# Performance work log

Measured on AMD Instinct MI355X. Metric: run time of the kernel, lower is better.

The kernel has to match this reference:

```python
import jax, jax.numpy as jnp
import numpy as np

L, D, H, FF, I, MAXREL = 6, 512, 8, 2048, 50, 128
HD = D // H
NREL = 2 * MAXREL + 1
EPS = 1e-5


def setup_inputs() -> dict:
    key = jax.random.key(0)
    ks = jax.random.split(key, 32)
    s = 0.02
    p = {
        'x': jax.random.normal(ks[0], (16, 512, I), dtype=jnp.float32),
        'in_w': jax.random.normal(ks[1], (I, D)) * s,
        'in_b': jnp.zeros((D,), jnp.float32),
        'Wq': jax.random.normal(ks[2], (L, D, D)) * s,
        'Wk': jax.random.normal(ks[3], (L, D, D)) * s,
        'Wv': jax.random.normal(ks[4], (L, D, D)) * s,
        'Wo': jax.random.normal(ks[5], (L, D, D)) * s,
        'bo': jnp.zeros((L, D), jnp.float32),
        'rel_emb': jax.random.normal(ks[6], (L, NREL, HD)) * s,
        'w1': jax.random.normal(ks[7], (L, D, FF)) * s,
        'b1': jnp.zeros((L, FF), jnp.float32),
        'w2': jax.random.normal(ks[8], (L, FF, D)) * s,
        'b2': jnp.zeros((L, D), jnp.float32),
        'ln1_g': jnp.ones((L, D), jnp.float32),
        'ln1_b': jnp.zeros((L, D), jnp.float32),
        'ln2_g': jnp.ones((L, D), jnp.float32),
        'ln2_b': jnp.zeros((L, D), jnp.float32),
        'on_g': jnp.ones((D,), jnp.float32),
        'on_b': jnp.zeros((D,), jnp.float32),
        'p1_w': jax.random.normal(ks[9], (D, D // 2)) * s,
        'p1_b': jnp.zeros((D // 2,), jnp.float32),
        'p2_w': jax.random.normal(ks[10], (D // 2, 1)) * s,
        'p2_b': jnp.zeros((1,), jnp.float32),
    }
    return p


def _layer_norm(x, g, b):
    m = jnp.mean(x, axis=-1, keepdims=True)
    v = jnp.mean(jnp.square(x - m), axis=-1, keepdims=True)
    return (x - m) * jax.lax.rsqrt(v + EPS) * g + b


def _sinusoidal_pe(seq_len, d_model):
    pos = jnp.arange(seq_len, dtype=jnp.float32)[:, None]
    div = jnp.exp(jnp.arange(0, d_model, 2, dtype=jnp.float32) * (-jnp.log(10000.0) / d_model))
    pe = jnp.zeros((seq_len, d_model), jnp.float32)
    pe = pe.at[:, 0::2].set(jnp.sin(pos * div))
    pe = pe.at[:, 1::2].set(jnp.cos(pos * div))
    return pe


def reference(x, in_w, in_b, Wq, Wk, Wv, Wo, bo, rel_emb, w1, b1, w2, b2,
              ln1_g, ln1_b, ln2_g, ln2_b, on_g, on_b, p1_w, p1_b, p2_w, p2_b):
    B, S, _ = x.shape
    scale = jnp.sqrt(jnp.float32(HD))
    # relative position index matrix [S, S] in [0, 2*MAXREL]
    r = jnp.arange(S)
    rel_idx = jnp.clip(r[None, :] - r[:, None], -MAXREL, MAXREL) + MAXREL

    h = x @ in_w + in_b                       # [B,S,D]
    h = h + _sinusoidal_pe(S, D)

    for l in range(L):
        q = (h @ Wq[l]).reshape(B, S, H, HD).transpose(0, 2, 1, 3)  # [B,H,S,hd]
        k = (h @ Wk[l]).reshape(B, S, H, HD).transpose(0, 2, 1, 3)
        v = (h @ Wv[l]).reshape(B, S, H, HD).transpose(0, 2, 1, 3)
        scores = jnp.einsum('bhqd,bhkd->bhqk', q, k) / scale
        rel = rel_emb[l][rel_idx]             # [S,S,hd]
        scores = scores + jnp.einsum('bhqd,qkd->bhqk', q, rel)  # rel bias is NOT scaled (matches source)
        attn = jax.nn.softmax(scores, axis=-1)
        ctx = jnp.einsum('bhqk,bhkd->bhqd', attn, v)
        ctx = ctx.transpose(0, 2, 1, 3).reshape(B, S, D)
        attn_out = ctx @ Wo[l] + bo[l]
        h = _layer_norm(h + attn_out, ln1_g[l], ln1_b[l])
        ff = jax.nn.relu(h @ w1[l] + b1[l]) @ w2[l] + b2[l]
        h = _layer_norm(h + ff, ln2_g[l], ln2_b[l])

    h = _layer_norm(h, on_g, on_b)
    out = jax.nn.relu(h @ p1_w + p1_b) @ p2_w + p2_b  # [B,S,1]
    return out
```

## Files before the change

### kernel.cpp

```cpp
#include <hip/hip_runtime.h>

typedef unsigned short u16;
typedef unsigned int   u32;
typedef short   short8  __attribute__((ext_vector_type(8)));
typedef float   floatx4 __attribute__((ext_vector_type(4)));

#define NTOK 8192
#define SEQ  512
#define NLAYER 6

#define OFF_WT   ((size_t)0)
#define OFF_HB   ((size_t)38010880)
#define OFF_QKV  ((size_t)46399488)
#define OFF_CTX  ((size_t)71565312)
#define OFF_GOUT ((size_t)79953920)
#define OFF_FF   ((size_t)96731136)
#define OFF_HD1  ((size_t)130285568)
#define OFF_VT   OFF_FF
#define OFF_RELB OFF_HD1

#define LSTRIDE 3145728
#define P1T_OFF 18874368

__device__ __forceinline__ float b2f(u16 v) { return __uint_as_float(((u32)v) << 16); }
__device__ __forceinline__ float lo16(u32 v) { return __uint_as_float(v << 16); }
__device__ __forceinline__ float hi16(u32 v) { return __uint_as_float(v & 0xffff0000u); }
__device__ __forceinline__ u16 f2b(float f) {
  u32 x = __float_as_uint(f);
  return (u16)((x + 0x7fffu + ((x >> 16) & 1u)) >> 16);
}
__device__ __forceinline__ u32 pack2(float a, float b) {
  return (u32)f2b(a) | ((u32)f2b(b) << 16);
}

typedef __attribute__((address_space(1))) void* gas_t;
typedef __attribute__((address_space(3))) void* las_t;

__global__ __launch_bounds__(256) void transpose_all(
    const float* __restrict__ Wq, const float* __restrict__ Wk,
    const float* __restrict__ Wv, const float* __restrict__ Wo,
    const float* __restrict__ w1, const float* __restrict__ w2,
    const float* __restrict__ p1, u16* __restrict__ wT)
{
  __shared__ u16 tile[64][65];
  const int tb = blockIdx.x;
  const float* src; u16* dst; int R, C, tidx;
  if (tb < 4608) {
    const int l = tb / 768, r = tb % 768;
    const size_t lofs = (size_t)l * LSTRIDE;
    if (r < 256) {
      const int m = r >> 6; tidx = r & 63; R = 512; C = 512;
      const float* bases[4] = {Wq, Wk, Wv, Wo};
      src = bases[m] + (size_t)l * 262144;
      dst = wT + lofs + (size_t)m * 262144;
    } else if (r < 512) {
      tidx = r - 256; R = 512; C = 2048;
      src = w1 + (size_t)l * 1048576; dst = wT + lofs + 1048576;
    } else {
      tidx = r - 512; R = 2048; C = 512;
      src = w2 + (size_t)l * 1048576; dst = wT + lofs + 2097152;
    }
  } else {
    tidx = tb - 4608; R = 512; C = 256;
    src = p1; dst = wT + P1T_OFF;
  }
  const int tcn = C >> 6;
  const int tr = tidx / tcn, tc = tidx % tcn;
  const int th = threadIdx.x;
  {
    const int lr = th >> 2, cg = (th & 3) * 16;
    const float* sp = src + (size_t)(tr*64 + lr) * C + tc*64 + cg;
    float4 f0 = *(const float4*)(sp);
    float4 f1 = *(const float4*)(sp + 4);
    float4 f2 = *(const float4*)(sp + 8);
    float4 f3 = *(const float4*)(sp + 12);
    u16* tp = &tile[lr][cg];
    tp[0]=f2b(f0.x); tp[1]=f2b(f0.y); tp[2]=f2b(f0.z); tp[3]=f2b(f0.w);
    tp[4]=f2b(f1.x); tp[5]=f2b(f1.y); tp[6]=f2b(f1.z); tp[7]=f2b(f1.w);
    tp[8]=f2b(f2.x); tp[9]=f2b(f2.y); tp[10]=f2b(f2.z); tp[11]=f2b(f2.w);
    tp[12]=f2b(f3.x); tp[13]=f2b(f3.y); tp[14]=f2b(f3.z); tp[15]=f2b(f3.w);
  }
  __syncthreads();
  {
    const int oc = th >> 2, rg = (th & 3) * 16;
    u32 wds[8];
    #pragma unroll
    for (int i = 0; i < 8; ++i)
      wds[i] = (u32)tile[rg + 2*i][oc] | ((u32)tile[rg + 2*i + 1][oc] << 16);
    u16* dp = dst + (size_t)(tc*64 + oc) * R + tr*64 + rg;
    uint4 o0; o0.x=wds[0]; o0.y=wds[1]; o0.z=wds[2]; o0.w=wds[3];
    uint4 o1; o1.x=wds[4]; o1.y=wds[5]; o1.z=wds[6]; o1.w=wds[7];
    *(uint4*)dp = o0;
    *(uint4*)(dp + 8) = o1;
  }
}

__global__ __launch_bounds__(128) void input_proj(
    const float* __restrict__ x, const float* __restrict__ w, const float* __restrict__ ib,
    u16* __restrict__ hb)
{
  const int row = blockIdx.x, t = threadIdx.x;
  const int s = row & (SEQ - 1);
  __shared__ float xs[50];
  if (t < 50) xs[t] = x[row*50 + t];
  __syncthreads();
  #pragma unroll
  for (int rep = 0; rep < 4; ++rep) {
    const int d = rep*128 + t;
    float acc = ib[d];
    #pragma unroll
    for (int i = 0; i < 50; ++i) acc += xs[i] * w[i*512 + d];
    const int ii = d >> 1;
    const float dv = __expf((float)(2*ii) * -0.017988946f);
    const float ang = (float)s * dv;
    const float pe = (d & 1) ? cosf(ang) : sinf(ang);
    hb[(size_t)row*512 + d] = f2b(acc + pe);
  }
}

__global__ __launch_bounds__(256) void gemm_bt(
    const u16* __restrict__ A, const u16* __restrict__ Bt,
    const float* __restrict__ bias,
    float* __restrict__ outF0, float* __restrict__ outF1, u16* __restrict__ outB,
    u16* __restrict__ vTout,
    const int M, const int N, const int K, const int kLen, const int flags)
{
  __shared__ __align__(16) u16 As[2*128*32];
  __shared__ __align__(16) u16 Bs[2*128*32];
  const int id = blockIdx.x;
  const int xcd = id & 7, rest = id >> 3;
  const int bm = (rest & 7) * 8 + xcd;
  const int bn = rest >> 3;
  const int z = blockIdx.y;
  const int kOff = z * kLen;
  const int m0 = bm << 7, n0 = bn << 7;
  const int tid = threadIdx.x;
  const int wave = tid >> 6, lane = tid & 63;
  const int wr = (wave >> 1) << 6, wc = (wave & 1) << 6;
  const int lrow = lane & 15, lquad = lane >> 4;

  floatx4 acc[4][4];
  #pragma unroll
  for (int i = 0; i < 4; ++i)
    #pragma unroll
    for (int j = 0; j < 4; ++j) { floatx4 zz = {0.f,0.f,0.f,0.f}; acc[i][j] = zz; }

  const u16* a0p = A  + (size_t)m0 * K + kOff;
  const u16* b0p = Bt + (size_t)n0 * K + kOff;
  const int c0 = tid, c1 = 256 + tid;
  const int ar0 = c0 >> 2, as0 = (c0 & 3) * 8;
  const int ar1 = c1 >> 2, as1 = (c1 & 3) * 8;

  for (int k0 = 0; k0 < kLen; k0 += 64) {
    #pragma unroll
    for (int hh = 0; hh < 2; ++hh) {
      const int kk = k0 + hh*32;
      __builtin_amdgcn_global_load_lds((gas_t)(a0p + (size_t)ar0*K + kk + as0), (las_t)(&As[hh*4096 + c0*8]), 16, 0, 0);
      __builtin_amdgcn_global_load_lds((gas_t)(a0p + (size_t)ar1*K + kk + as1), (las_t)(&As[hh*4096 + c1*8]), 16, 0, 0);
      __builtin_amdgcn_global_load_lds((gas_t)(b0p + (size_t)ar0*K + kk + as0), (las_t)(&Bs[hh*4096 + c0*8]), 16, 0, 0);
      __builtin_amdgcn_global_load_lds((gas_t)(b0p + (size_t)ar1*K + kk + as1), (las_t)(&Bs[hh*4096 + c1*8]), 16, 0, 0);
    }
    __syncthreads();
    #pragma unroll
    for (int hh = 0; hh < 2; ++hh) {
      short8 af[4], bf[4];
      #pragma unroll
      for (int i = 0; i < 4; ++i) af[i] = *(const short8*)&As[hh*4096 + (wr + i*16 + lrow)*32 + lquad*8];
      #pragma unroll
      for (int j = 0; j < 4; ++j) bf[j] = *(const short8*)&Bs[hh*4096 + (wc + j*16 + lrow)*32 + lquad*8];
      #pragma unroll
      for (int i = 0; i < 4; ++i)
        #pragma unroll
        for (int j = 0; j < 4; ++j)
          acc[i][j] = __builtin_amdgcn_mfma_f32_16x16x32_bf16(bf[j], af[i], acc[i][j], 0, 0, 0);
    }
    __syncthreads();
  }

  if ((flags & 4) && n0 >= 1024) {
    #pragma unroll
    for (int i = 0; i < 4; ++i) {
      const int row = m0 + wr + i*16 + lrow;
      const int bb = row >> 9, s = row & 511;
      #pragma unroll
      for (int j = 0; j < 4; ++j) {
        const int cm0 = (n0 - 1024) + wc + j*16 + lquad*4;
        #pragma unroll
        for (int v = 0; v < 4; ++v) {
          const int cm = cm0 + v;
          const int hh = cm >> 6, d = cm & 63;
          vTout[((size_t)(bb*8 + hh)*64 + d)*512 + s] = f2b(acc[i][j][v]);
        }
      }
    }
    return;
  }

  float* outF = (z == 0) ? outF0 : outF1;
  const bool hasb = ((flags & 1) != 0) && (z == 0);
  const bool dorelu = (flags & 2) != 0;
  #pragma unroll
  for (int i = 0; i < 4; ++i) {
    const int row = m0 + wr + i*16 + lrow;
    #pragma unroll
    for (int j = 0; j < 4; ++j) {
      const int colbase = n0 + wc + j*16 + lquad*4;
      float4 bv4 = make_float4(0.f, 0.f, 0.f, 0.f);
      if (hasb) bv4 = *(const float4*)(bias + colbase);
      float v0 = acc[i][j][0] + bv4.x;
      float v1 = acc[i][j][1] + bv4.y;
      float v2 = acc[i][j][2] + bv4.z;
      float v3 = acc[i][j][3] + bv4.w;
      if (dorelu) {
        v0 = fmaxf(v0, 0.f); v1 = fmaxf(v1, 0.f);
        v2 = fmaxf(v2, 0.f); v3 = fmaxf(v3, 0.f);
      }
      const size_t off = (size_t)row * N + colbase;
      if (outB) {
        uint2 o; o.x = pack2(v0, v1); o.y = pack2(v2, v3);
        *(uint2*)(outB + off) = o;
      } else {
        *(float4*)(outF + off) = make_float4(v0, v1, v2, v3);
      }
    }
  }
}

__global__ __launch_bounds__(256) void cvt_rel_all(
    const float* __restrict__ rel, u16* __restrict__ relB)
{
  const int i = blockIdx.x*256 + threadIdx.x;
  if (i < 6*257*64) {
    const int l = i / 16448, rem = i % 16448;
    relB[l*17408 + rem] = f2b(rel[i]);
  }
}

__global__ __launch_bounds__(256) void attn_mfma(
    const u16* __restrict__ qkv, const u16* __restrict__ vT,
    const u16* __restrict__ relB, u16* __restrict__ ctx)
{
  const int id = blockIdx.x;
  const int xcd = id & 7, g = (id >> 3) & 15, qt = id >> 7;
  const int bh = xcd*16 + g;
  const int b = bh >> 3, h = bh & 7;
  const int t = threadIdx.x, w = t >> 6, lane = t & 63;
  const int lr = lane & 15, quad = lane >> 4;

  __shared__ __align__(16) u16 Ks[64*72];
  __shared__ __align__(16) u16 Vs[64*72];
  __shared__ __align__(16) u16 Pr[64*280];

  const size_t token0 = (size_t)b*512 + qt*64;

  short8 af0, af1;
  {
    const u16* qp = qkv + (token0 + w*16 + lr)*1536 + h*64 + quad*8;
    af0 = *(const short8*)(qp);
    af1 = *(const short8*)(qp + 32);
  }

  #pragma unroll 4
  for (int nt = 0; nt < 17; ++nt) {
    const u16* rp = relB + (nt*16 + lr)*64 + quad*8;
    short8 rb0 = *(const short8*)(rp);
    short8 rb1 = *(const short8*)(rp + 32);
    floatx4 c = {0.f,0.f,0.f,0.f};
    c = __builtin_amdgcn_mfma_f32_16x16x32_bf16(af0, rb0, c, 0, 0, 0);
    c = __builtin_amdgcn_mfma_f32_16x16x32_bf16(af1, rb1, c, 0, 0, 0);
    #pragma unroll
    for (int r = 0; r < 4; ++r)
      Pr[(w*16 + quad*4 + r)*280 + nt*16 + lr] = f2b(c[r]);
  }

  floatx4 oacc[4];
  floatx4 lacc = {0.f,0.f,0.f,0.f};
  #pragma unroll
  for (int n = 0; n < 4; ++n) { floatx4 zz = {0.f,0.f,0.f,0.f}; oacc[n] = zz; }

  short8 ones;
  #pragma unroll
  for (int i = 0; i < 8; ++i) ones[i] = (short)0x3F80;

  const int srow = t >> 2, scol = (t & 3) * 16;
  const u16* kbase = qkv + (size_t)b*512*1536 + 512 + h*64;
  const u16* vbase = vT + (size_t)(b*8 + h)*64*512;
  const int qg0 = qt*64 + w*16 + quad*4;

  for (int kt = 0; kt < 8; ++kt) {
    __syncthreads();
    {
      const u16* kp = kbase + (size_t)(kt*64 + srow)*1536 + scol;
      uint4 k0 = *(const uint4*)kp;
      uint4 k1 = *(const uint4*)(kp + 8);
      const u16* vp = vbase + (size_t)srow*512 + kt*64 + scol;
      uint4 v0 = *(const uint4*)vp;
      uint4 v1 = *(const uint4*)(vp + 8);
      *(uint4*)&Ks[srow*72 + scol]     = k0;
      *(uint4*)&Ks[srow*72 + scol + 8] = k1;
      *(uint4*)&Vs[srow*72 + scol]     = v0;
      *(uint4*)&Vs[srow*72 + scol + 8] = v1;
    }
    __syncthreads();

    floatx4 s4[4];
    #pragma unroll
    for (int nt = 0; nt < 4; ++nt) {
      short8 kb0 = *(const short8*)&Ks[(nt*16 + lr)*72 + quad*8];
      short8 kb1 = *(const short8*)&Ks[(nt*16 + lr)*72 + 32 + quad*8];
      floatx4 c = {0.f,0.f,0.f,0.f};
      c = __builtin_amdgcn_mfma_f32_16x16x32_bf16(af0, kb0, c, 0, 0, 0);
      c = __builtin_amdgcn_mfma_f32_16x16x32_bf16(af1, kb1, c, 0, 0, 0);
      s4[nt] = c;
    }
    __syncthreads();

    const int kpos = kt*64 + lr;
    #pragma unroll
    for (int r = 0; r < 4; ++r) {
      const int qg = qg0 + r;
      const int prrow = (w*16 + quad*4 + r)*280;
      const int psrow = (w*16 + quad*4 + r)*72;
      #pragma unroll
      for (int nt = 0; nt < 4; ++nt) {
        int dd = (kpos + nt*16) - qg;
        dd = dd < -128 ? -128 : (dd > 128 ? 128 : dd);
        const float sc = fmaf(s4[nt][r], 0.125f, b2f(Pr[prrow + dd + 128]));
        Ks[psrow + nt*16 + lr] = f2b(__expf(sc));
      }
    }

    short8 pf0 = *(const short8*)&Ks[(w*16 + lr)*72 + quad*8];
    short8 pf1 = *(const short8*)&Ks[(w*16 + lr)*72 + 32 + quad*8];
    lacc = __builtin_amdgcn_mfma_f32_16x16x32_bf16(ones, pf0, lacc, 0, 0, 0);
    lacc = __builtin_amdgcn_mfma_f32_16x16x32_bf16(ones, pf1, lacc, 0, 0, 0);
    #pragma unroll
    for (int nd = 0; nd < 4; ++nd) {
      short8 vb0 = *(const short8*)&Vs[(nd*16 + lr)*72 + quad*8];
      short8 vb1 = *(const short8*)&Vs[(nd*16 + lr)*72 + 32 + quad*8];
      oacc[nd] = __builtin_amdgcn_mfma_f32_16x16x32_bf16(vb0, pf0, oacc[nd], 0, 0, 0);
      oacc[nd] = __builtin_amdgcn_mfma_f32_16x16x32_bf16(vb1, pf1, oacc[nd], 0, 0, 0);
    }
  }

  {
    const float inv = 1.f / lacc[0];
    u16* cp = ctx + (token0 + w*16 + lr)*512 + h*64;
    #pragma unroll
    for (int nd = 0; nd < 4; ++nd) {
      const int d = nd*16 + quad*4;
      uint2 o;
      o.x = pack2(oacc[nd][0]*inv, oacc[nd][1]*inv);
      o.y = pack2(oacc[nd][2]*inv, oacc[nd][3]*inv);
      *(uint2*)(cp + d) = o;
    }
  }
}

__global__ __launch_bounds__(128) void ln_kernel(
    const u16* __restrict__ resB, const float* __restrict__ add0,
    const float* __restrict__ add1,
    const float* __restrict__ g, const float* __restrict__ be,
    u16* __restrict__ hb)
{
  const int row = blockIdx.x, t = threadIdx.x;
  const size_t base = (size_t)row * 512;
  const u32 r0 = *(const u32*)(resB + base + t*4);
  const u32 r1 = *(const u32*)(resB + base + t*4 + 2);
  float x0 = lo16(r0), x1 = hi16(r0), x2 = lo16(r1), x3 = hi16(r1);
  if (add0) {
    const float4 a = *(const float4*)(add0 + base + t*4);
    x0 += a.x; x1 += a.y; x2 += a.z; x3 += a.w;
  }
  if (add1) {
    const float4 a = *(const float4*)(add1 + base + t*4);
    x0 += a.x; x1 += a.y; x2 += a.z; x3 += a.w;
  }
  float s = x0 + x1 + x2 + x3;
  #pragma unroll
  for (int off = 32; off > 0; off >>= 1) s += __shfl_down(s, off);
  __shared__ float red[2];
  const int wv = t >> 6, ln = t & 63;
  if (ln == 0) red[wv] = s;
  __syncthreads();
  const float mean = (red[0] + red[1]) * (1.f/512.f);
  const float dx0 = x0-mean, dx1 = x1-mean, dx2 = x2-mean, dx3 = x3-mean;
  float vs = dx0*dx0 + dx1*dx1 + dx2*dx2 + dx3*dx3;
  __syncthreads();
  #pragma unroll
  for (int off = 32; off > 0; off >>= 1) vs += __shfl_down(vs, off);
  if (ln == 0) red[wv] = vs;
  __syncthreads();
  const float var = (red[0] + red[1]) * (1.f/512.f);
  const float inv = 1.f / sqrtf(var + 1e-5f);
  const float4 gv = *(const float4*)(g + t*4);
  const float4 bv = *(const float4*)(be + t*4);
  const float y0 = dx0*inv*gv.x + bv.x;
  const float y1 = dx1*inv*gv.y + bv.y;
  const float y2 = dx2*inv*gv.z + bv.z;
  const float y3 = dx3*inv*gv.w + bv.w;
  u32* hp = (u32*)(hb + base + t*4);
  hp[0] = pack2(y0, y1); hp[1] = pack2(y2, y3);
}

__global__ __launch_bounds__(256) void head2_kernel(
    const u16* __restrict__ hd1, const float* __restrict__ p2w,
    const float* __restrict__ p2b, float* __restrict__ out)
{
  const int wv = threadIdx.x >> 6, ln = threadIdx.x & 63;
  const int row = blockIdx.x * 4 + wv;
  const u16* hp = hd1 + (size_t)row * 256 + ln*4;
  const u32 h0 = *(const u32*)hp, h1 = *(const u32*)(hp + 2);
  const float4 w = *(const float4*)(p2w + ln*4);
  float acc = lo16(h0)*w.x + hi16(h0)*w.y + lo16(h1)*w.z + hi16(h1)*w.w;
  #pragma unroll
  for (int off = 1; off < 64; off <<= 1) acc += __shfl_xor(acc, off);
  if (ln == 0) out[row] = acc + p2b[0];
}

extern "C" void kernel_launch(void* const* d_in, const int* in_sizes, int n_in,
                              void* d_out, int out_size, void* d_ws, size_t ws_size,
                              hipStream_t stream) {
  (void)in_sizes; (void)n_in; (void)out_size; (void)ws_size;
  const float* X    = (const float*)d_in[0];
  const float* INW  = (const float*)d_in[1];
  const float* INB  = (const float*)d_in[2];
  const float* WQ   = (const float*)d_in[3];
  const float* WK   = (const float*)d_in[4];
  const float* WV   = (const float*)d_in[5];
  const float* WO   = (const float*)d_in[6];
  const float* BO   = (const float*)d_in[7];
  const float* REL  = (const float*)d_in[8];
  const float* W1   = (const float*)d_in[9];
  const float* B1   = (const float*)d_in[10];
  const float* W2   = (const float*)d_in[11];
  const float* B2   = (const float*)d_in[12];
  const float* LN1G = (const float*)d_in[13];
  const float* LN1B = (const float*)d_in[14];
  const float* LN2G = (const float*)d_in[15];
  const float* LN2B = (const float*)d_in[16];
  const float* ONG  = (const float*)d_in[17];
  const float* ONB  = (const float*)d_in[18];
  const float* P1W  = (const float*)d_in[19];
  const float* P1B  = (const float*)d_in[20];
  const float* P2W  = (const float*)d_in[21];
  const float* P2B  = (const float*)d_in[22];
  float* out = (float*)d_out;

  char* ws = (char*)d_ws;
  u16*   wT    = (u16*)(ws + OFF_WT);
  u16*   hB    = (u16*)(ws + OFF_HB);
  u16*   qkv   = (u16*)(ws + OFF_QKV);
  u16*   ctx   = (u16*)(ws + OFF_CTX);
  float* gout0 = (float*)(ws + OFF_GOUT);
  float* gout1 = (float*)(ws + OFF_QKV);
  u16*   ff    = (u16*)(ws + OFF_FF);
  u16*   hd1   = (u16*)(ws + OFF_HD1);
  u16*   vTb   = (u16*)(ws + OFF_VT);
  u16*   relBa = (u16*)(ws + OFF_RELB);

  transpose_all<<<4640, 256, 0, stream>>>(WQ, WK, WV, WO, W1, W2, P1W, wT);
  cvt_rel_all<<<386, 256, 0, stream>>>(REL, relBa);
  input_proj<<<NTOK, 128, 0, stream>>>(X, INW, INB, hB);

  for (int l = 0; l < NLAYER; ++l) {
    const u16* wTl = wT + (size_t)l * LSTRIDE;
    gemm_bt<<<dim3(768,1), 256, 0, stream>>>(hB, wTl, nullptr, nullptr, nullptr, qkv, vTb,
                                             8192, 1536, 512, 512, 4);
    attn_mfma<<<1024, 256, 0, stream>>>(qkv, vTb, relBa + l*17408, ctx);
    gemm_bt<<<dim3(256,2), 256, 0, stream>>>(ctx, wTl + 786432, BO + l*512,
                                             gout0, gout1, nullptr, nullptr,
                                             8192, 512, 512, 256, 1);
    ln_kernel<<<NTOK, 128, 0, stream>>>(hB, gout0, gout1, LN1G + l*512, LN1B + l*512, hB);
    gemm_bt<<<dim3(1024,1), 256, 0, stream>>>(hB, wTl + 1048576, B1 + l*2048,
                                              nullptr, nullptr, ff, nullptr,
                                              8192, 2048, 512, 512, 3);
    gemm_bt<<<dim3(256,2), 256, 0, stream>>>(ff, wTl + 2097152, B2 + l*512,
                                             gout0, gout1, nullptr, nullptr,
                                             8192, 512, 2048, 1024, 1);
    ln_kernel<<<NTOK, 128, 0, stream>>>(hB, gout0, gout1, LN2G + l*512, LN2B + l*512, hB);
  }
  ln_kernel<<<NTOK, 128, 0, stream>>>(hB, nullptr, nullptr, ONG, ONB, hB);
  gemm_bt<<<dim3(128,1), 256, 0, stream>>>(hB, wT + P1T_OFF, P1B,
                                           nullptr, nullptr, hd1, nullptr,
                                           8192, 256, 512, 512, 3);
  head2_kernel<<<2048, 256, 0, stream>>>(hd1, P2W, P2B, out);
}
```

Before: 1.184 ms.

## Load K/V fragments directly from global in attention, drop LDS staging and barriers

After: 1.454 ms. 1.23x slower.

```diff
diff --git a/kernel.cpp b/kernel.cpp
--- a/kernel.cpp
+++ b/kernel.cpp
@@ -236,7 +236,7 @@
   }
 }
 
-__global__ __launch_bounds__(256) void attn_mfma(
+__global__ __launch_bounds__(256, 3) void attn_mfma(
     const u16* __restrict__ qkv, const u16* __restrict__ vT,
     const u16* __restrict__ relB, u16* __restrict__ ctx)
 {
@@ -247,9 +247,8 @@
   const int t = threadIdx.x, w = t >> 6, lane = t & 63;
   const int lr = lane & 15, quad = lane >> 4;
 
-  __shared__ __align__(16) u16 Ks[64*72];
-  __shared__ __align__(16) u16 Vs[64*72];
-  __shared__ __align__(16) u16 Pr[64*280];
+  __shared__ __align__(16) u16 Pr[64*272];
+  __shared__ __align__(16) u16 Ps[64*68];
 
   const size_t token0 = (size_t)b*512 + qt*64;
 
@@ -270,7 +269,7 @@
     c = __builtin_amdgcn_mfma_f32_16x16x32_bf16(af1, rb1, c, 0, 0, 0);
     #pragma unroll
     for (int r = 0; r < 4; ++r)
-      Pr[(w*16 + quad*4 + r)*280 + nt*16 + lr] = f2b(c[r]);
+      Pr[(w*16 + quad*4 + r)*272 + nt*16 + lr] = f2b(c[r] * 1.44269504f);
   }
 
   floatx4 oacc[4];
@@ -282,64 +281,60 @@
   #pragma unroll
   for (int i = 0; i < 8; ++i) ones[i] = (short)0x3F80;
 
-  const int srow = t >> 2, scol = (t & 3) * 16;
   const u16* kbase = qkv + (size_t)b*512*1536 + 512 + h*64;
-  const u16* vbase = vT + (size_t)(b*8 + h)*64*512;
+  const u16* vbase = vT + (size_t)bh*64*512;
   const int qg0 = qt*64 + w*16 + quad*4;
-
+  const int prrow0 = (w*16 + quad*4)*272;
+  const int psrow0 = (w*16 + quad*4)*68;
+
+  #pragma unroll 1
   for (int kt = 0; kt < 8; ++kt) {
-    __syncthreads();
-    {
-      const u16* kp = kbase + (size_t)(kt*64 + srow)*1536 + scol;
-      uint4 k0 = *(const uint4*)kp;
-      uint4 k1 = *(const uint4*)(kp + 8);
-      const u16* vp = vbase + (size_t)srow*512 + kt*64 + scol;
-      uint4 v0 = *(const uint4*)vp;
-      uint4 v1 = *(const uint4*)(vp + 8);
-      *(uint4*)&Ks[srow*72 + scol]     = k0;
-      *(uint4*)&Ks[srow*72 + scol + 8] = k1;
-      *(uint4*)&Vs[srow*72 + scol]     = v0;
-      *(uint4*)&Vs[srow*72 + scol + 8] = v1;
-    }
-    __syncthreads();
+    short8 kb0[4], kb1[4], vb0[4], vb1[4];
+    #pragma unroll
+    for (int nt = 0; nt < 4; ++nt) {
+      const u16* kp = kbase + (size_t)(kt*64 + nt*16 + lr)*1536 + quad*8;
+      kb0[nt] = *(const short8*)(kp);
+      kb1[nt] = *(const short8*)(kp + 32);
+    }
+    #pragma unroll
+    for (int nd = 0; nd < 4; ++nd) {
+      const u16* vp = vbase + (size_t)(nd*16 + lr)*512 + kt*64 + quad*8;
+      vb0[nd] = *(const short8*)(vp);
+      vb1[nd] = *(const short8*)(vp + 32);
+    }
 
     floatx4 s4[4];
     #pragma unroll
     for (int nt = 0; nt < 4; ++nt) {
-      short8 kb0 = *(const short8*)&Ks[(nt*16 + lr)*72 + quad*8];
-      short8 kb1 = *(const short8*)&Ks[(nt*16 + lr)*72 + 32 + quad*8];
       floatx4 c = {0.f,0.f,0.f,0.f};
-      c = __builtin_amdgcn_mfma_f32_16x16x32_bf16(af0, kb0, c, 0, 0, 0);
-      c = __builtin_amdgcn_mfma_f32_16x16x32_bf16(af1, kb1, c, 0, 0, 0);
+      c = __builtin_amdgcn_mfma_f32_16x16x32_bf16(af0, kb0[nt], c, 0, 0, 0);
+      c = __builtin_amdgcn_mfma_f32_16x16x32_bf16(af1, kb1[nt], c, 0, 0, 0);
       s4[nt] = c;
     }
-    __syncthreads();
 
     const int kpos = kt*64 + lr;
     #pragma unroll
     for (int r = 0; r < 4; ++r) {
       const int qg = qg0 + r;
-      const int prrow = (w*16 + quad*4 + r)*280;
-      const int psrow = (w*16 + quad*4 + r)*72;
+      const int prrow = prrow0 + r*272;
+      const int psrow = psrow0 + r*68;
       #pragma unroll
       for (int nt = 0; nt < 4; ++nt) {
         int dd = (kpos + nt*16) - qg;
         dd = dd < -128 ? -128 : (dd > 128 ? 128 : dd);
-        const float sc = fmaf(s4[nt][r], 0.125f, b2f(Pr[prrow + dd + 128]));
-        Ks[psrow + nt*16 + lr] = f2b(__expf(sc));
+        const float sc = fmaf(s4[nt][r], 0.18033688f, b2f(Pr[prrow + dd + 128]));
+        Ps[psrow + nt*16 + lr] = f2b(exp2f(sc));
       }
     }
 
-    short8 pf0 = *(const short8*)&Ks[(w*16 + lr)*72 + quad*8];
-    short8 pf1 = *(const short8*)&Ks[(w*16 + lr)*72 + 32 + quad*8];
+    short8 pf0 = *(const short8*)&Ps[(w*16 + lr)*68 + quad*8];
+    short8 pf1 = *(const short8*)&Ps[(w*16 + lr)*68 + 32 + quad*8];
     lacc = __builtin_amdgcn_mfma_f32_16x16x32_bf16(ones, pf0, lacc, 0, 0, 0);
     lacc = __builtin_amdgcn_mfma_f32_16x16x32_bf16(ones, pf1, lacc, 0, 0, 0);
     #pragma unroll
     for (int nd = 0; nd < 4; ++nd) {
-      short8 vb0 = *(const short8*)&Vs[(nd*16 + lr)*72 + quad*8];
-      short8 vb1 = *(const short8*)&Vs[(nd*16 + lr)*72 + 32 + quad*8];
-      oacc[nd] = __builtin_amdgcn_mfma_f32_16x16x32_bf16(vb0, pf0, oacc[nd], 0, 0, 0);
-      oacc[nd] = __builtin_amdgcn_mfma_f32_16x16x32_bf16(vb1, pf1, oacc[nd], 0, 0, 0);
+      oacc[nd] = __builtin_amdgcn_mfma_f32_16x16x32_bf16(vb0[nd], pf0, oacc[nd], 0, 0, 0);
+      oacc[nd] = __builtin_amdgcn_mfma_f32_16x16x32_bf16(vb1[nd], pf1, oacc[nd], 0, 0, 0);
     }
   }
 
```

## Prefetch next K/V tile into registers and use exp2 in attention

Applied to the files above, without the earlier changes.

Measured after the change: 1.178 ms. About the same (-0.5%).

```diff
diff --git a/kernel.cpp b/kernel.cpp
--- a/kernel.cpp
+++ b/kernel.cpp
@@ -236,7 +236,7 @@
   }
 }
 
-__global__ __launch_bounds__(256) void attn_mfma(
+__global__ __launch_bounds__(256, 3) void attn_mfma(
     const u16* __restrict__ qkv, const u16* __restrict__ vT,
     const u16* __restrict__ relB, u16* __restrict__ ctx)
 {
@@ -249,15 +249,26 @@
 
   __shared__ __align__(16) u16 Ks[64*72];
   __shared__ __align__(16) u16 Vs[64*72];
-  __shared__ __align__(16) u16 Pr[64*280];
+  __shared__ __align__(16) u16 Pr[64*272];
 
   const size_t token0 = (size_t)b*512 + qt*64;
+  const int srow = t >> 2, scol = (t & 3) * 16;
+  const u16* kbase = qkv + (size_t)b*512*1536 + 512 + h*64;
+  const u16* vbase = vT + (size_t)bh*64*512;
 
   short8 af0, af1;
   {
     const u16* qp = qkv + (token0 + w*16 + lr)*1536 + h*64 + quad*8;
     af0 = *(const short8*)(qp);
     af1 = *(const short8*)(qp + 32);
+  }
+
+  uint4 kr0, kr1, vr0, vr1;
+  {
+    const u16* kp = kbase + (size_t)srow*1536 + scol;
+    kr0 = *(const uint4*)kp; kr1 = *(const uint4*)(kp + 8);
+    const u16* vp = vbase + (size_t)srow*512 + scol;
+    vr0 = *(const uint4*)vp; vr1 = *(const uint4*)(vp + 8);
   }
 
   #pragma unroll 4
@@ -270,7 +281,7 @@
     c = __builtin_amdgcn_mfma_f32_16x16x32_bf16(af1, rb1, c, 0, 0, 0);
     #pragma unroll
     for (int r = 0; r < 4; ++r)
-      Pr[(w*16 + quad*4 + r)*280 + nt*16 + lr] = f2b(c[r]);
+      Pr[(w*16 + quad*4 + r)*272 + nt*16 + lr] = f2b(c[r] * 1.44269504f);
   }
 
   floatx4 oacc[4];
@@ -282,28 +293,27 @@
   #pragma unroll
   for (int i = 0; i < 8; ++i) ones[i] = (short)0x3F80;
 
-  const int srow = t >> 2, scol = (t & 3) * 16;
-  const u16* kbase = qkv + (size_t)b*512*1536 + 512 + h*64;
-  const u16* vbase = vT + (size_t)(b*8 + h)*64*512;
   const int qg0 = qt*64 + w*16 + quad*4;
+  const int prrow0 = (w*16 + quad*4)*272;
+  const int psrow0 = (w*16 + quad*4)*72;
 
   for (int kt = 0; kt < 8; ++kt) {
     __syncthreads();
-    {
-      const u16* kp = kbase + (size_t)(kt*64 + srow)*1536 + scol;
-      uint4 k0 = *(const uint4*)kp;
-      uint4 k1 = *(const uint4*)(kp + 8);
-      const u16* vp = vbase + (size_t)srow*512 + kt*64 + scol;
-      uint4 v0 = *(const uint4*)vp;
-      uint4 v1 = *(const uint4*)(vp + 8);
-      *(uint4*)&Ks[srow*72 + scol]     = k0;
-      *(uint4*)&Ks[srow*72 + scol + 8] = k1;
-      *(uint4*)&Vs[srow*72 + scol]     = v0;
-      *(uint4*)&Vs[srow*72 + scol + 8] = v1;
-    }
+    *(uint4*)&Ks[srow*72 + scol]     = kr0;
+    *(uint4*)&Ks[srow*72 + scol + 8] = kr1;
+    *(uint4*)&Vs[srow*72 + scol]     = vr0;
+    *(uint4*)&Vs[srow*72 + scol + 8] = vr1;
     __syncthreads();
 
+    if (kt < 7) {
+      const u16* kp = kbase + (size_t)((kt+1)*64 + srow)*1536 + scol;
+      kr0 = *(const uint4*)kp; kr1 = *(const uint4*)(kp + 8);
+      const u16* vp = vbase + (size_t)srow*512 + (kt+1)*64 + scol;
+      vr0 = *(const uint4*)vp; vr1 = *(const uint4*)(vp + 8);
+    }
+
     floatx4 s4[4];
+    __builtin_amdgcn_s_setprio(1);
     #pragma unroll
     for (int nt = 0; nt < 4; ++nt) {
       short8 kb0 = *(const short8*)&Ks[(nt*16 + lr)*72 + quad*8];
@@ -313,25 +323,27 @@
       c = __builtin_amdgcn_mfma_f32_16x16x32_bf16(af1, kb1, c, 0, 0, 0);
       s4[nt] = c;
     }
+    __builtin_amdgcn_s_setprio(0);
     __syncthreads();
 
     const int kpos = kt*64 + lr;
     #pragma unroll
     for (int r = 0; r < 4; ++r) {
       const int qg = qg0 + r;
-      const int prrow = (w*16 + quad*4 + r)*280;
-      const int psrow = (w*16 + quad*4 + r)*72;
+      const int prrow = prrow0 + r*272;
+      const int psrow = psrow0 + r*72;
       #pragma unroll
       for (int nt = 0; nt < 4; ++nt) {
         int dd = (kpos + nt*16) - qg;
         dd = dd < -128 ? -128 : (dd > 128 ? 128 : dd);
-        const float sc = fmaf(s4[nt][r], 0.125f, b2f(Pr[prrow + dd + 128]));
-        Ks[psrow + nt*16 + lr] = f2b(__expf(sc));
+        const float sc = fmaf(s4[nt][r], 0.18033688f, b2f(Pr[prrow + dd + 128]));
+        Ks[psrow + nt*16 + lr] = f2b(exp2f(sc));
       }
     }
 
     short8 pf0 = *(const short8*)&Ks[(w*16 + lr)*72 + quad*8];
     short8 pf1 = *(const short8*)&Ks[(w*16 + lr)*72 + 32 + quad*8];
+    __builtin_amdgcn_s_setprio(1);
     lacc = __builtin_amdgcn_mfma_f32_16x16x32_bf16(ones, pf0, lacc, 0, 0, 0);
     lacc = __builtin_amdgcn_mfma_f32_16x16x32_bf16(ones, pf1, lacc, 0, 0, 0);
     #pragma unroll
@@ -341,6 +353,7 @@
       oacc[nd] = __builtin_amdgcn_mfma_f32_16x16x32_bf16(vb0, pf0, oacc[nd], 0, 0, 0);
       oacc[nd] = __builtin_amdgcn_mfma_f32_16x16x32_bf16(vb1, pf1, oacc[nd], 0, 0, 0);
     }
+    __builtin_amdgcn_s_setprio(0);
   }
 
   {
```
